# Kernel tuning notes

Measured on AMD Instinct MI355X. Metric: run time of the kernel, lower is better.

## Reference

```python
import jax, jax.numpy as jnp
import numpy as np

VOCAB = 32000
N = 4096        # reservoir_size
D = 32          # avg nonzeros per row -> density D/N
R_OUT = 512
BATCH = 8
T = 256
NNZ = N * D     # W_rec nonzeros = N*N*(D/N)


def setup_inputs() -> dict:
    key = jax.random.key(0)
    ks = jax.random.split(key, 9)
    x = jax.random.randint(ks[0], (BATCH, T), 0, VOCAB)
    # dense input table; sparse.mm(W_in_T, one_hot) == row gather W_in[x_t]
    W_in = jax.random.normal(ks[1], (VOCAB, N), jnp.float32)
    rec_rows = jax.random.randint(ks[2], (NNZ,), 0, N, dtype=jnp.int32)
    rec_cols = jax.random.randint(ks[3], (NNZ,), 0, N, dtype=jnp.int32)
    # small scale stands in for spectral-radius normalization (init-time detail)
    rec_vals = jax.random.normal(ks[4], (NNZ,), jnp.float32) * 0.05
    a = jax.random.uniform(ks[5], (N,), jnp.float32)  # leak rates in [0,1)
    B_w = jax.random.normal(ks[6], (R_OUT, N), jnp.float32) / np.sqrt(N)
    A_w = jax.random.normal(ks[7], (VOCAB, R_OUT), jnp.float32) / np.sqrt(R_OUT)
    A_b = jnp.zeros((VOCAB,), jnp.float32)
    return dict(x=x, W_in=W_in, rec_rows=rec_rows, rec_cols=rec_cols,
                rec_vals=rec_vals, a=a, B_w=B_w, A_w=A_w, A_b=A_b)


def reference(x, W_in, rec_rows, rec_cols, rec_vals, a, B_w, A_w, A_b):
    B = x.shape[0]

    def step(h, x_t):
        # input projection: one-hot @ W_in  ==  row gather
        u = W_in[x_t]                                   # (B, N)
        # sparse COO matvec: rec = W_rec @ h^T, batched over B
        contrib = rec_vals[None, :] * h[:, rec_cols]    # (B, nnz)
        rec = jnp.zeros_like(h).at[:, rec_rows].add(contrib)
        pre = jnp.clip(u + rec, -10.0, 10.0)
        h_new = (1.0 - a) * h + a * jnp.tanh(pre)
        out = (h_new @ B_w.T) @ A_w.T + A_b             # (B, vocab)
        return h_new, out

    h0 = jnp.zeros((B, W_in.shape[1]), W_in.dtype)
    _, outs = jax.lax.scan(step, h0, x.T)               # (T, B, V)
    return jnp.transpose(outs, (1, 0, 2))               # (B, T, V)
```

## Files before the change

kernel.cpp:

```cpp
#include <hip/hip_runtime.h>
#include <hip/hip_bf16.h>
#include <stdint.h>

#define N_RES 4096
#define BATCH 8
#define T_STEPS 256
#define VOCAB 32000
#define R_OUT 512
#define NNZ 131072
#define NNZ_CAP 163840
#define TEAMS 8
#define SLICES 16
#define ROWS_PS 256
#define NWG (TEAMS*SLICES)
#define CSR_CAP 10240

typedef _Float16 v8h __attribute__((ext_vector_type(8)));
typedef float v4f __attribute__((ext_vector_type(4)));

static __device__ __forceinline__ unsigned short f2h(float f) {
    _Float16 h = (_Float16)f;
    unsigned short u;
    __builtin_memcpy(&u, &h, 2);
    return u;
}
static __device__ __forceinline__ float h2f(unsigned short u) {
    _Float16 h;
    __builtin_memcpy(&h, &u, 2);
    return (float)h;
}


#define FLAG_WORDS (TEAMS * SLICES * 32)
#define INIT_WORDS (NNZ_CAP + 4096 + FLAG_WORDS)

__global__ __launch_bounds__(256) void k_init(unsigned* __restrict__ csr,
                                              int* __restrict__ cnt,
                                              unsigned* __restrict__ flags) {
    int i = blockIdx.x * 256 + threadIdx.x;
    if (i < NNZ_CAP) csr[i] = 0u;
    else if (i < NNZ_CAP + 4096) cnt[i - NNZ_CAP] = 0;
    else if (i < INIT_WORDS) flags[i - NNZ_CAP - 4096] = 0u;
}


__global__ __launch_bounds__(256) void k_hist(const int* __restrict__ rows,
                                              int* __restrict__ cnt) {
    int i = blockIdx.x * 256 + threadIdx.x;
    if (i < NNZ) atomicAdd(&cnt[rows[i]], 1);
}

__global__ __launch_bounds__(1024) void k_scan(const int* __restrict__ cnt,
                                               int* __restrict__ row_ptr,
                                               int* __restrict__ cursor) {
    __shared__ int sm[1024];
    int t = threadIdx.x;
    int base = t * 4;
    int c0 = (cnt[base] + 7) & ~7;
    int c1 = (cnt[base + 1] + 7) & ~7;
    int c2 = (cnt[base + 2] + 7) & ~7;
    int c3 = (cnt[base + 3] + 7) & ~7;
    int s = c0 + c1 + c2 + c3;
    sm[t] = s;
    __syncthreads();
    for (int off = 1; off < 1024; off <<= 1) {
        int v = (t >= off) ? sm[t - off] : 0;
        __syncthreads();
        sm[t] += v;
        __syncthreads();
    }
    int run = sm[t] - s;
    row_ptr[base] = run;     cursor[base] = run;     run += c0;
    row_ptr[base + 1] = run; cursor[base + 1] = run; run += c1;
    row_ptr[base + 2] = run; cursor[base + 2] = run; run += c2;
    row_ptr[base + 3] = run; cursor[base + 3] = run; run += c3;
    if (t == 1023) row_ptr[4096] = run;
}

__global__ __launch_bounds__(256) void k_fill(const int* __restrict__ rows,
                                              const int* __restrict__ cols,
                                              const float* __restrict__ vals,
                                              int* __restrict__ cursor,
                                              unsigned* __restrict__ csr) {
    int i = blockIdx.x * 256 + threadIdx.x;
    if (i < NNZ) {
        int r = rows[i];
        int c = cols[i];
        int p = atomicAdd(&cursor[r], 1);
        unsigned off = ((unsigned)(c & 15) << 10) | ((unsigned)(c >> 4) << 2);
        csr[p] = (off << 16) | (unsigned)f2h(vals[i]);
    }
}


#define NB8 (R_OUT * N_RES / 8)
#define NA8 (VOCAB * R_OUT / 8)

__global__ __launch_bounds__(256) void k_cvt2(const float* __restrict__ Bw,
                                              unsigned short* __restrict__ Bwh,
                                              const float* __restrict__ Aw,
                                              unsigned short* __restrict__ Awh) {
    int i = blockIdx.x * 256 + threadIdx.x;
    const float* src;
    unsigned short* dst;
    int j;
    if (i < NB8) { src = Bw; dst = Bwh; j = i * 8; }
    else if (i < NB8 + NA8) { src = Aw; dst = Awh; j = (i - NB8) * 8; }
    else return;
    float4 a0 = *reinterpret_cast<const float4*>(src + j);
    float4 a1 = *reinterpret_cast<const float4*>(src + j + 4);
    unsigned short o[8] = { f2h(a0.x), f2h(a0.y), f2h(a0.z), f2h(a0.w),
                            f2h(a1.x), f2h(a1.y), f2h(a1.z), f2h(a1.w) };
    *reinterpret_cast<uint4*>(dst + j) = *reinterpret_cast<const uint4*>(o);
}


__global__ __launch_bounds__(256) void k_steps(const int* __restrict__ rowptr,
                                               const unsigned* __restrict__ csr,
                                               const float* __restrict__ W_in,
                                               const int* __restrict__ x,
                                               const float* __restrict__ a,
                                               unsigned short* __restrict__ Hb,
                                               unsigned long long* __restrict__ hx,
                                               unsigned* __restrict__ flags) {
    __shared__ float plane[4096];
    __shared__ __align__(16) unsigned lcsr[CSR_CAP];
    __shared__ unsigned long long stage64[64];
    __shared__ int ltok[T_STEPS];

    int wg = blockIdx.x;
    int tid = threadIdx.x;
    int team = wg & 7;
    int slice = wg >> 3;
    int r_own = slice * ROWS_PS + tid;

    ltok[tid] = x[team * T_STEPS + tid];

    int j0 = rowptr[slice * ROWS_PS];
    int j1 = rowptr[slice * ROWS_PS + ROWS_PS];
    int cntE = j1 - j0;
    if (cntE > CSR_CAP) cntE = CSR_CAP;
    {
        const uint4* src = reinterpret_cast<const uint4*>(csr + j0);
        int n4 = cntE >> 2;
        for (int k = tid; k < n4; k += 256)
            reinterpret_cast<uint4*>(lcsr)[k] = src[k];
    }
    for (int k = tid; k < 4096; k += 256) plane[k] = 0.f;

    int js = rowptr[r_own] - j0;
    int je = rowptr[r_own + 1] - j0;
    if (js > CSR_CAP) js = CSR_CAP;
    if (je > CSR_CAP) je = CSR_CAP;
    float av = a[r_own];
    float oma = 1.f - av;
    int pown = ((r_own & 15) << 8) | (r_own >> 4);
    __syncthreads();

    float u_cur = W_in[(size_t)ltok[0] * N_RES + r_own];

    for (int t = 0; t < T_STEPS; ++t) {
        float u_nxt = 0.f;
        if (t + 1 < T_STEPS)
            u_nxt = W_in[(size_t)ltok[t + 1] * N_RES + r_own];

        float acc = 0.f;
        for (int j = js; j < je; j += 8) {
            uint4 e0 = *reinterpret_cast<const uint4*>(lcsr + j);
            uint4 e1 = *reinterpret_cast<const uint4*>(lcsr + j + 4);
            unsigned ee[8] = { e0.x, e0.y, e0.z, e0.w, e1.x, e1.y, e1.z, e1.w };
#pragma unroll
            for (int q = 0; q < 8; ++q) {
                float g = *reinterpret_cast<const float*>(
                    reinterpret_cast<const char*>(plane) + (ee[q] >> 16));
                acc += h2f((unsigned short)(ee[q] & 0xffffu)) * g;
            }
        }
        float hold = plane[pown];
        float pre = u_cur + acc;
        pre = fminf(fmaxf(pre, -10.f), 10.f);
        float ex = __expf(2.f * pre);
        float th = 1.f - 2.f / (ex + 1.f);
        float hv = oma * hold + av * th;
        unsigned short hv16 = f2h(hv);
        Hb[((size_t)(team * T_STEPS + t) << 12) + r_own] = hv16;
        u_cur = u_nxt;

        if (t == T_STEPS - 1) break;

        reinterpret_cast<unsigned short*>(stage64)[tid] = hv16;
        __syncthreads();
        int par = t & 1;
        unsigned long long* base = hx + ((size_t)(par * TEAMS + team)) * 1024;
        if (tid < 64) {
            unsigned long long d = stage64[tid];
            __hip_atomic_store(base + slice * 64 + tid, d,
                               __ATOMIC_RELAXED, __HIP_MEMORY_SCOPE_AGENT);
        }
        asm volatile("s_waitcnt vmcnt(0)" ::: "memory");
        __syncthreads();
        if (tid == 0)
            __hip_atomic_store(flags + (team * SLICES + slice) * 32, (unsigned)(t + 1),
                               __ATOMIC_RELAXED, __HIP_MEMORY_SCOPE_AGENT);
        if (tid < SLICES) {
            const unsigned* fp = flags + (team * SLICES + tid) * 32;
            while (__hip_atomic_load(fp, __ATOMIC_RELAXED,
                                     __HIP_MEMORY_SCOPE_AGENT) < (unsigned)(t + 1)) {}
        }
        __syncthreads();
        const unsigned long long* src = base + tid * 4;
#pragma unroll
        for (int k = 0; k < 4; ++k) {
            unsigned long long d = __hip_atomic_load(src + k, __ATOMIC_RELAXED,
                                                     __HIP_MEMORY_SCOPE_AGENT);
            int jb = k * 4;
            plane[((jb + 0) << 8) | tid] = h2f((unsigned short)(d & 0xffffu));
            plane[((jb + 1) << 8) | tid] = h2f((unsigned short)((d >> 16) & 0xffffu));
            plane[((jb + 2) << 8) | tid] = h2f((unsigned short)((d >> 32) & 0xffffu));
            plane[((jb + 3) << 8) | tid] = h2f((unsigned short)((d >> 48) & 0xffffu));
        }
        __syncthreads();
    }
}


static __device__ __forceinline__ void stage128x32(const _Float16* __restrict__ g,
                                                   int ld, int row0, int k0,
                                                   _Float16* lds, int wave, int lane) {
#pragma unroll
    for (int q = 0; q < 2; ++q) {
        int i = wave * 128 + q * 64 + lane;
        const _Float16* src = g + (size_t)(row0 + (i >> 2)) * ld + k0 + (i & 3) * 8;
        int loff = __builtin_amdgcn_readfirstlane((wave * 128 + q * 64) * 16);
        __builtin_amdgcn_global_load_lds(
            (const __attribute__((address_space(1))) void*)src,
            (__attribute__((address_space(3))) void*)((char*)lds + loff),
            16, 0, 0);
    }
}


__global__ __launch_bounds__(256) void k_gemm1(const _Float16* __restrict__ Hb,
                                               const _Float16* __restrict__ Bwh,
                                               unsigned short* __restrict__ Rbh) {
    __shared__ _Float16 As[2][128 * 32];
    __shared__ _Float16 Bs[2][128 * 32];
    int tid = threadIdx.x, lane = tid & 63, wave = tid >> 6;
    int wm = wave >> 1, wn = wave & 1;
    int col0 = blockIdx.x * 128;
    int row0 = blockIdx.y * 128;
    int rA = lane & 15, kA = (lane >> 4) * 8;
    v4f acc[4][4];
#pragma unroll
    for (int s = 0; s < 4; ++s)
#pragma unroll
        for (int f = 0; f < 4; ++f) acc[s][f] = (v4f){0.f, 0.f, 0.f, 0.f};

    stage128x32(Hb,  N_RES, row0, 0, As[0], wave, lane);
    stage128x32(Bwh, N_RES, col0, 0, Bs[0], wave, lane);
    const int NIT = N_RES / 32;
    for (int it = 0; it < NIT; ++it) {
        int cur = it & 1;
        __syncthreads();
        asm volatile("s_waitcnt vmcnt(0)" ::: "memory");
        __syncthreads();
        if (it + 1 < NIT) {
            stage128x32(Hb,  N_RES, row0, (it + 1) * 32, As[cur ^ 1], wave, lane);
            stage128x32(Bwh, N_RES, col0, (it + 1) * 32, Bs[cur ^ 1], wave, lane);
        }
        v8h af[4], bf[4];
#pragma unroll
        for (int s = 0; s < 4; ++s)
            af[s] = *reinterpret_cast<const v8h*>(&As[cur][(wm * 64 + s * 16 + rA) * 32 + kA]);
#pragma unroll
        for (int f = 0; f < 4; ++f)
            bf[f] = *reinterpret_cast<const v8h*>(&Bs[cur][(wn * 64 + f * 16 + rA) * 32 + kA]);
#pragma unroll
        for (int s = 0; s < 4; ++s)
#pragma unroll
            for (int f = 0; f < 4; ++f)
                acc[s][f] = __builtin_amdgcn_mfma_f32_16x16x32_f16(af[s], bf[f], acc[s][f], 0, 0, 0);
    }
#pragma unroll
    for (int f = 0; f < 4; ++f) {
        int col = col0 + wn * 64 + f * 16 + (lane & 15);
#pragma unroll
        for (int s = 0; s < 4; ++s)
#pragma unroll
            for (int r = 0; r < 4; ++r) {
                int row = row0 + wm * 64 + s * 16 + (lane >> 4) * 4 + r;
                Rbh[(size_t)row * R_OUT + col] = f2h(acc[s][f][r]);
            }
    }
}


__global__ __launch_bounds__(256) void k_gemm2(const _Float16* __restrict__ Rbh,
                                               const _Float16* __restrict__ Awh,
                                               const float* __restrict__ Ab,
                                               float* __restrict__ out) {
    __shared__ _Float16 As[2][128 * 32];
    __shared__ _Float16 Bs[2][128 * 32];
    int tid = threadIdx.x, lane = tid & 63, wave = tid >> 6;
    int wm = wave >> 1, wn = wave & 1;
    int col0 = blockIdx.x * 128;
    int row0 = blockIdx.y * 128;
    int rA = lane & 15, kA = (lane >> 4) * 8;
    v4f acc[4][4];
#pragma unroll
    for (int s = 0; s < 4; ++s)
#pragma unroll
        for (int f = 0; f < 4; ++f) acc[s][f] = (v4f){0.f, 0.f, 0.f, 0.f};

    stage128x32(Rbh, R_OUT, row0, 0, As[0], wave, lane);
    stage128x32(Awh, R_OUT, col0, 0, Bs[0], wave, lane);
    const int NIT = R_OUT / 32;
    for (int it = 0; it < NIT; ++it) {
        int cur = it & 1;
        __syncthreads();
        asm volatile("s_waitcnt vmcnt(0)" ::: "memory");
        __syncthreads();
        if (it + 1 < NIT) {
            stage128x32(Rbh, R_OUT, row0, (it + 1) * 32, As[cur ^ 1], wave, lane);
            stage128x32(Awh, R_OUT, col0, (it + 1) * 32, Bs[cur ^ 1], wave, lane);
        }
        v8h af[4], bf[4];
#pragma unroll
        for (int s = 0; s < 4; ++s)
            af[s] = *reinterpret_cast<const v8h*>(&As[cur][(wm * 64 + s * 16 + rA) * 32 + kA]);
#pragma unroll
        for (int f = 0; f < 4; ++f)
            bf[f] = *reinterpret_cast<const v8h*>(&Bs[cur][(wn * 64 + f * 16 + rA) * 32 + kA]);
#pragma unroll
        for (int s = 0; s < 4; ++s)
#pragma unroll
            for (int f = 0; f < 4; ++f)
                acc[s][f] = __builtin_amdgcn_mfma_f32_16x16x32_f16(af[s], bf[f], acc[s][f], 0, 0, 0);
    }
#pragma unroll
    for (int f = 0; f < 4; ++f) {
        float bias = Ab[col0 + wn * 64 + f * 16 + (lane & 15)];
#pragma unroll
        for (int s = 0; s < 4; ++s)
#pragma unroll
            for (int r = 0; r < 4; ++r) acc[s][f][r] += bias;
    }
    float* Ct = (float*)As;
#pragma unroll
    for (int s = 0; s < 4; ++s) {
        __syncthreads();
#pragma unroll
        for (int f = 0; f < 4; ++f) {
            int lc = wn * 64 + f * 16 + (lane & 15);
            int lr = wm * 16 + (lane >> 4) * 4;
#pragma unroll
            for (int r = 0; r < 4; ++r)
                Ct[(lr + r) * 128 + lc] = acc[s][f][r];
        }
        __syncthreads();
        int lr2 = tid >> 3;
        int lc2 = (tid & 7) * 16;
        int grow = row0 + (lr2 & 15) + (lr2 >> 4) * 64 + s * 16;
        float* dst = out + (size_t)grow * VOCAB + col0 + lc2;
        const float* srcl = &Ct[lr2 * 128 + lc2];
#pragma unroll
        for (int v = 0; v < 4; ++v)
            *reinterpret_cast<float4*>(dst + v * 4) =
                *reinterpret_cast<const float4*>(srcl + v * 4);
    }
}


extern "C" void kernel_launch(void* const* d_in, const int* in_sizes, int n_in,
                              void* d_out, int out_size, void* d_ws, size_t ws_size,
                              hipStream_t stream) {
    const int*   x        = (const int*)d_in[0];
    const float* W_in     = (const float*)d_in[1];
    const int*   rec_rows = (const int*)d_in[2];
    const int*   rec_cols = (const int*)d_in[3];
    const float* rec_vals = (const float*)d_in[4];
    const float* a        = (const float*)d_in[5];
    const float* B_w      = (const float*)d_in[6];
    const float* A_w      = (const float*)d_in[7];
    const float* A_b      = (const float*)d_in[8];
    float* out = (float*)d_out;

    char* w = (char*)d_ws;
    size_t off = 0;
    auto alloc = [&](size_t bytes) { void* p = w + off; off = (off + bytes + 255) & ~(size_t)255; return p; };

    unsigned short* Hb     = (unsigned short*)alloc((size_t)2048 * N_RES * 2);
    unsigned short* Rbh    = (unsigned short*)alloc((size_t)2048 * R_OUT * 2);
    unsigned short* Bwh    = (unsigned short*)alloc((size_t)R_OUT * N_RES * 2);
    unsigned short* Awh    = (unsigned short*)alloc((size_t)VOCAB * R_OUT * 2);
    unsigned*       csr    = (unsigned*)alloc((size_t)NNZ_CAP * 4);
    int*            rowptr = (int*)alloc(4097 * 4);
    int*            cnt    = (int*)alloc(4096 * 4);
    int*            cursor = (int*)alloc(4096 * 4);
    unsigned long long* hx = (unsigned long long*)alloc(2 * TEAMS * 1024 * 8);
    unsigned*       flags  = (unsigned*)alloc(FLAG_WORDS * 4);

    k_init<<<(INIT_WORDS + 255) / 256, 256, 0, stream>>>(csr, cnt, flags);

    k_hist<<<(NNZ + 255) / 256, 256, 0, stream>>>(rec_rows, cnt);
    k_scan<<<1, 1024, 0, stream>>>(cnt, rowptr, cursor);
    k_fill<<<(NNZ + 255) / 256, 256, 0, stream>>>(rec_rows, rec_cols, rec_vals, cursor, csr);

    k_cvt2<<<(NB8 + NA8 + 255) / 256, 256, 0, stream>>>(B_w, Bwh, A_w, Awh);

    k_steps<<<NWG, 256, 0, stream>>>(rowptr, csr, W_in, x, a, Hb, hx, flags);

    k_gemm1<<<dim3(R_OUT / 128, 2048 / 128), 256, 0, stream>>>(
        (const _Float16*)Hb, (const _Float16*)Bwh, Rbh);
    k_gemm2<<<dim3(VOCAB / 128, 2048 / 128), 256, 0, stream>>>(
        (const _Float16*)Rbh, (const _Float16*)Awh, A_b, out);
}
```

Baseline: 1.342 ms.

## Replace flag barrier with epoch-tagged per-element exchange and XCD-local team mapping

Removes the per-step flag store/spin barrier and staging through LDS. Each thread instead publishes its h value tagged with the step epoch into two buffers: one written at workgroup scope and polled with sc0 loads, and one written at agent scope that serves as a fallback after repeated polling failures. Workgroups are remapped so a team's slices are contiguous block IDs, presumably to place them on the same XCD and share its L2, and the plane layout becomes linear. The fast path depends on hardware scheduling placing a team's blocks on one XCD, so correctness of the workgroup-scope path leans on that placement and on the fallback.

```diff
diff --git a/kernel.cpp b/kernel.cpp
--- a/kernel.cpp
+++ b/kernel.cpp
@@ -31,16 +31,18 @@
 }
 
 
-#define FLAG_WORDS (TEAMS * SLICES * 32)
-#define INIT_WORDS (NNZ_CAP + 4096 + FLAG_WORDS)
+#define HX_WORDS (2 * TEAMS * 4096)
+#define INIT_WORDS (NNZ_CAP + 4096 + 2 * HX_WORDS)
 
 __global__ __launch_bounds__(256) void k_init(unsigned* __restrict__ csr,
                                               int* __restrict__ cnt,
-                                              unsigned* __restrict__ flags) {
+                                              unsigned* __restrict__ hxL,
+                                              unsigned* __restrict__ hxG) {
     int i = blockIdx.x * 256 + threadIdx.x;
     if (i < NNZ_CAP) csr[i] = 0u;
     else if (i < NNZ_CAP + 4096) cnt[i - NNZ_CAP] = 0;
-    else if (i < INIT_WORDS) flags[i - NNZ_CAP - 4096] = 0u;
+    else if (i < NNZ_CAP + 4096 + HX_WORDS) hxL[i - NNZ_CAP - 4096] = 0u;
+    else if (i < INIT_WORDS) hxG[i - NNZ_CAP - 4096 - HX_WORDS] = 0u;
 }
 
 
@@ -85,9 +87,8 @@
     int i = blockIdx.x * 256 + threadIdx.x;
     if (i < NNZ) {
         int r = rows[i];
-        int c = cols[i];
+        unsigned off = (unsigned)(cols[i] << 2);
         int p = atomicAdd(&cursor[r], 1);
-        unsigned off = ((unsigned)(c & 15) << 10) | ((unsigned)(c >> 4) << 2);
         csr[p] = (off << 16) | (unsigned)f2h(vals[i]);
     }
 }
@@ -121,19 +122,20 @@
                                                const int* __restrict__ x,
                                                const float* __restrict__ a,
                                                unsigned short* __restrict__ Hb,
-                                               unsigned long long* __restrict__ hx,
-                                               unsigned* __restrict__ flags) {
+                                               unsigned* __restrict__ hxL,
+                                               unsigned* __restrict__ hxG) {
     __shared__ float plane[4096];
     __shared__ __align__(16) unsigned lcsr[CSR_CAP];
-    __shared__ unsigned long long stage64[64];
     __shared__ int ltok[T_STEPS];
+    __shared__ int s_fb;
 
     int wg = blockIdx.x;
     int tid = threadIdx.x;
-    int team = wg & 7;
-    int slice = wg >> 3;
+    int team = wg >> 4;
+    int slice = wg & 15;
     int r_own = slice * ROWS_PS + tid;
 
+    if (tid == 0) s_fb = 0;
     ltok[tid] = x[team * T_STEPS + tid];
 
     int j0 = rowptr[slice * ROWS_PS];
@@ -154,7 +156,6 @@
     if (je > CSR_CAP) je = CSR_CAP;
     float av = a[r_own];
     float oma = 1.f - av;
-    int pown = ((r_own & 15) << 8) | (r_own >> 4);
     __syncthreads();
 
     float u_cur = W_in[(size_t)ltok[0] * N_RES + r_own];
@@ -176,7 +177,7 @@
                 acc += h2f((unsigned short)(ee[q] & 0xffffu)) * g;
             }
         }
-        float hold = plane[pown];
+        float hold = plane[r_own];
         float pre = u_cur + acc;
         pre = fminf(fmaxf(pre, -10.f), 10.f);
         float ex = __expf(2.f * pre);
@@ -188,36 +189,76 @@
 
         if (t == T_STEPS - 1) break;
 
-        reinterpret_cast<unsigned short*>(stage64)[tid] = hv16;
-        __syncthreads();
-        int par = t & 1;
-        unsigned long long* base = hx + ((size_t)(par * TEAMS + team)) * 1024;
-        if (tid < 64) {
-            unsigned long long d = stage64[tid];
-            __hip_atomic_store(base + slice * 64 + tid, d,
-                               __ATOMIC_RELAXED, __HIP_MEMORY_SCOPE_AGENT);
-        }
-        asm volatile("s_waitcnt vmcnt(0)" ::: "memory");
-        __syncthreads();
-        if (tid == 0)
-            __hip_atomic_store(flags + (team * SLICES + slice) * 32, (unsigned)(t + 1),
-                               __ATOMIC_RELAXED, __HIP_MEMORY_SCOPE_AGENT);
-        if (tid < SLICES) {
-            const unsigned* fp = flags + (team * SLICES + tid) * 32;
-            while (__hip_atomic_load(fp, __ATOMIC_RELAXED,
-                                     __HIP_MEMORY_SCOPE_AGENT) < (unsigned)(t + 1)) {}
-        }
-        __syncthreads();
-        const unsigned long long* src = base + tid * 4;
-#pragma unroll
-        for (int k = 0; k < 4; ++k) {
-            unsigned long long d = __hip_atomic_load(src + k, __ATOMIC_RELAXED,
-                                                     __HIP_MEMORY_SCOPE_AGENT);
-            int jb = k * 4;
-            plane[((jb + 0) << 8) | tid] = h2f((unsigned short)(d & 0xffffu));
-            plane[((jb + 1) << 8) | tid] = h2f((unsigned short)((d >> 16) & 0xffffu));
-            plane[((jb + 2) << 8) | tid] = h2f((unsigned short)((d >> 32) & 0xffffu));
-            plane[((jb + 3) << 8) | tid] = h2f((unsigned short)((d >> 48) & 0xffffu));
+        unsigned e = (unsigned)(t + 1);
+        size_t pofs = (((size_t)(e & 1u) * TEAMS + team) << 12);
+        unsigned tagged = (e << 16) | (unsigned)hv16;
+
+        __hip_atomic_store(hxL + pofs + r_own, tagged,
+                           __ATOMIC_RELAXED, __HIP_MEMORY_SCOPE_WORKGROUP);
+        __hip_atomic_store(hxG + pofs + r_own, tagged,
+                           __ATOMIC_RELAXED, __HIP_MEMORY_SCOPE_AGENT);
+
+        unsigned long long g[8];
+        bool fb = (s_fb != 0);
+#define TAGOK64(v) ((((unsigned)((v) >> 16) & 0xffffu) == e) && ((unsigned)((v) >> 48) == e))
+        if (!fb) {
+            uint4 q0, q1, q2, q3;
+            const char* pL = reinterpret_cast<const char*>(hxL + pofs) + (size_t)tid * 64;
+            int tries = 0;
+            for (;;) {
+                asm volatile("global_load_dwordx4 %0, %1, off sc0"
+                             : "=v"(q0) : "v"(pL) : "memory");
+                asm volatile("global_load_dwordx4 %0, %1, off offset:16 sc0"
+                             : "=v"(q1) : "v"(pL) : "memory");
+                asm volatile("global_load_dwordx4 %0, %1, off offset:32 sc0"
+                             : "=v"(q2) : "v"(pL) : "memory");
+                asm volatile("global_load_dwordx4 %0, %1, off offset:48 sc0"
+                             : "=v"(q3) : "v"(pL) : "memory");
+                asm volatile("s_waitcnt vmcnt(0)" ::: "memory");
+                g[0] = (unsigned long long)q0.x | ((unsigned long long)q0.y << 32);
+                g[1] = (unsigned long long)q0.z | ((unsigned long long)q0.w << 32);
+                g[2] = (unsigned long long)q1.x | ((unsigned long long)q1.y << 32);
+                g[3] = (unsigned long long)q1.z | ((unsigned long long)q1.w << 32);
+                g[4] = (unsigned long long)q2.x | ((unsigned long long)q2.y << 32);
+                g[5] = (unsigned long long)q2.z | ((unsigned long long)q2.w << 32);
+                g[6] = (unsigned long long)q3.x | ((unsigned long long)q3.y << 32);
+                g[7] = (unsigned long long)q3.z | ((unsigned long long)q3.w << 32);
+                bool ok = true;
+#pragma unroll
+                for (int k = 0; k < 8; ++k) ok = ok && TAGOK64(g[k]);
+                if (ok) break;
+                if (++tries > 256) { fb = true; s_fb = 1; break; }
+            }
+        }
+        if (fb) {
+            const unsigned long long* xG64 =
+                reinterpret_cast<const unsigned long long*>(hxG + pofs) + (size_t)tid * 8;
+#pragma unroll
+            for (int k = 0; k < 8; ++k)
+                g[k] = __hip_atomic_load(xG64 + k, __ATOMIC_RELAXED,
+                                         __HIP_MEMORY_SCOPE_AGENT);
+            for (;;) {
+                unsigned m = 0;
+#pragma unroll
+                for (int k = 0; k < 8; ++k)
+                    m |= TAGOK64(g[k]) ? 0u : (1u << k);
+                if (!m) break;
+#pragma unroll
+                for (int k = 0; k < 8; ++k)
+                    if (m & (1u << k))
+                        g[k] = __hip_atomic_load(xG64 + k, __ATOMIC_RELAXED,
+                                                 __HIP_MEMORY_SCOPE_AGENT);
+            }
+        }
+#undef TAGOK64
+
+        __syncthreads();
+#pragma unroll
+        for (int k = 0; k < 8; ++k) {
+            float2 v;
+            v.x = h2f((unsigned short)(g[k] & 0xffffu));
+            v.y = h2f((unsigned short)((g[k] >> 32) & 0xffffu));
+            *reinterpret_cast<float2*>(&plane[16 * tid + 2 * k]) = v;
         }
         __syncthreads();
     }
@@ -397,10 +438,10 @@
     int*            rowptr = (int*)alloc(4097 * 4);
     int*            cnt    = (int*)alloc(4096 * 4);
     int*            cursor = (int*)alloc(4096 * 4);
-    unsigned long long* hx = (unsigned long long*)alloc(2 * TEAMS * 1024 * 8);
-    unsigned*       flags  = (unsigned*)alloc(FLAG_WORDS * 4);
-
-    k_init<<<(INIT_WORDS + 255) / 256, 256, 0, stream>>>(csr, cnt, flags);
+    unsigned*       hxL    = (unsigned*)alloc((size_t)HX_WORDS * 4);
+    unsigned*       hxG    = (unsigned*)alloc((size_t)HX_WORDS * 4);
+
+    k_init<<<(INIT_WORDS + 255) / 256, 256, 0, stream>>>(csr, cnt, hxL, hxG);
 
     k_hist<<<(NNZ + 255) / 256, 256, 0, stream>>>(rec_rows, cnt);
     k_scan<<<1, 1024, 0, stream>>>(cnt, rowptr, cursor);
@@ -408,7 +449,7 @@
 
     k_cvt2<<<(NB8 + NA8 + 255) / 256, 256, 0, stream>>>(B_w, Bwh, A_w, Awh);
 
-    k_steps<<<NWG, 256, 0, stream>>>(rowptr, csr, W_in, x, a, Hb, hx, flags);
+    k_steps<<<NWG, 256, 0, stream>>>(rowptr, csr, W_in, x, a, Hb, hxL, hxG);
 
     k_gemm1<<<dim3(R_OUT / 128, 2048 / 128), 256, 0, stream>>>(
         (const _Float16*)Hb, (const _Float16*)Bwh, Rbh);
```

Result: slower. 1.787 ms (+33.2%).

## Tag exchanged hidden state with epoch and shrink gemm1 tiles

Applied to the files above, without the earlier changes.

The recurrent step exchange now writes each element as a 32-bit word that packs an epoch tag with the fp16 value, straight from every thread. This drops the LDS staging, the vmcnt drain and one barrier before the flag store. Readers use sc0 sc1 dwordx4 loads and retry until every tag matches the current epoch, with an atomic fallback after a bounded number of retries. The exchange buffer doubles in size and the plane layout is remapped to match. Separately, gemm1 tiles shrink from 128x128 to 64x64, giving 256 workgroups instead of 64 so more CUs are busy, at the cost of less data reuse per tile.

```diff
diff --git a/kernel.cpp b/kernel.cpp
--- a/kernel.cpp
+++ b/kernel.cpp
@@ -121,11 +121,10 @@
                                                const int* __restrict__ x,
                                                const float* __restrict__ a,
                                                unsigned short* __restrict__ Hb,
-                                               unsigned long long* __restrict__ hx,
+                                               unsigned* __restrict__ hx,
                                                unsigned* __restrict__ flags) {
     __shared__ float plane[4096];
     __shared__ __align__(16) unsigned lcsr[CSR_CAP];
-    __shared__ unsigned long long stage64[64];
     __shared__ int ltok[T_STEPS];
 
     int wg = blockIdx.x;
@@ -183,42 +182,84 @@
         float th = 1.f - 2.f / (ex + 1.f);
         float hv = oma * hold + av * th;
         unsigned short hv16 = f2h(hv);
+
+        if (t == T_STEPS - 1) {
+            Hb[((size_t)(team * T_STEPS + t) << 12) + r_own] = hv16;
+            break;
+        }
+
+        unsigned e = (unsigned)(t + 1);
+        unsigned* xb = hx + (((size_t)(e & 1u) * TEAMS + team) << 12);
+
+        __hip_atomic_store(xb + r_own, (e << 16) | (unsigned)hv16,
+                           __ATOMIC_RELAXED, __HIP_MEMORY_SCOPE_AGENT);
+        __syncthreads();
+        if (tid == 0)
+            __hip_atomic_store(flags + (team * SLICES + slice) * 32, e,
+                               __ATOMIC_RELAXED, __HIP_MEMORY_SCOPE_AGENT);
+
         Hb[((size_t)(team * T_STEPS + t) << 12) + r_own] = hv16;
-        u_cur = u_nxt;
-
-        if (t == T_STEPS - 1) break;
-
-        reinterpret_cast<unsigned short*>(stage64)[tid] = hv16;
-        __syncthreads();
-        int par = t & 1;
-        unsigned long long* base = hx + ((size_t)(par * TEAMS + team)) * 1024;
-        if (tid < 64) {
-            unsigned long long d = stage64[tid];
-            __hip_atomic_store(base + slice * 64 + tid, d,
-                               __ATOMIC_RELAXED, __HIP_MEMORY_SCOPE_AGENT);
-        }
-        asm volatile("s_waitcnt vmcnt(0)" ::: "memory");
-        __syncthreads();
-        if (tid == 0)
-            __hip_atomic_store(flags + (team * SLICES + slice) * 32, (unsigned)(t + 1),
-                               __ATOMIC_RELAXED, __HIP_MEMORY_SCOPE_AGENT);
+
         if (tid < SLICES) {
             const unsigned* fp = flags + (team * SLICES + tid) * 32;
             while (__hip_atomic_load(fp, __ATOMIC_RELAXED,
-                                     __HIP_MEMORY_SCOPE_AGENT) < (unsigned)(t + 1)) {}
-        }
-        __syncthreads();
-        const unsigned long long* src = base + tid * 4;
-#pragma unroll
-        for (int k = 0; k < 4; ++k) {
-            unsigned long long d = __hip_atomic_load(src + k, __ATOMIC_RELAXED,
-                                                     __HIP_MEMORY_SCOPE_AGENT);
-            int jb = k * 4;
-            plane[((jb + 0) << 8) | tid] = h2f((unsigned short)(d & 0xffffu));
-            plane[((jb + 1) << 8) | tid] = h2f((unsigned short)((d >> 16) & 0xffffu));
-            plane[((jb + 2) << 8) | tid] = h2f((unsigned short)((d >> 32) & 0xffffu));
-            plane[((jb + 3) << 8) | tid] = h2f((unsigned short)((d >> 48) & 0xffffu));
-        }
+                                     __HIP_MEMORY_SCOPE_AGENT) < e) {}
+        }
+        __syncthreads();
+
+        uint4 v0, v1, v2, v3;
+        const char* p0 = reinterpret_cast<const char*>(xb) + (size_t)tid * 16;
+        const char* p1 = p0 + 4096;
+        const char* p2 = p0 + 8192;
+        const char* p3 = p0 + 12288;
+        asm volatile(
+            "global_load_dwordx4 %0, %4, off sc0 sc1\n\t"
+            "global_load_dwordx4 %1, %5, off sc0 sc1\n\t"
+            "global_load_dwordx4 %2, %6, off sc0 sc1\n\t"
+            "global_load_dwordx4 %3, %7, off sc0 sc1\n\t"
+            "s_waitcnt vmcnt(0)"
+            : "=&v"(v0), "=&v"(v1), "=&v"(v2), "=&v"(v3)
+            : "v"(p0), "v"(p1), "v"(p2), "v"(p3)
+            : "memory");
+#define QOK(v) (((v.x >> 16) == e) && ((v.y >> 16) == e) && \
+                ((v.z >> 16) == e) && ((v.w >> 16) == e))
+        int tries = 0;
+        while (!(QOK(v0) && QOK(v1) && QOK(v2) && QOK(v3)) && tries <= 64) {
+            ++tries;
+            if (!QOK(v0)) asm volatile("global_load_dwordx4 %0, %1, off sc0 sc1\n\ts_waitcnt vmcnt(0)" : "=&v"(v0) : "v"(p0) : "memory");
+            if (!QOK(v1)) asm volatile("global_load_dwordx4 %0, %1, off sc0 sc1\n\ts_waitcnt vmcnt(0)" : "=&v"(v1) : "v"(p1) : "memory");
+            if (!QOK(v2)) asm volatile("global_load_dwordx4 %0, %1, off sc0 sc1\n\ts_waitcnt vmcnt(0)" : "=&v"(v2) : "v"(p2) : "memory");
+            if (!QOK(v3)) asm volatile("global_load_dwordx4 %0, %1, off sc0 sc1\n\ts_waitcnt vmcnt(0)" : "=&v"(v3) : "v"(p3) : "memory");
+        }
+        if (tries > 64) {
+            unsigned w[16];
+#pragma unroll
+            for (int k = 0; k < 16; ++k) {
+                const unsigned* wp = xb + (k >> 2) * 1024 + tid * 4 + (k & 3);
+                unsigned g = __hip_atomic_load(wp, __ATOMIC_RELAXED, __HIP_MEMORY_SCOPE_AGENT);
+                while ((g >> 16) != e)
+                    g = __hip_atomic_load(wp, __ATOMIC_RELAXED, __HIP_MEMORY_SCOPE_AGENT);
+                w[k] = g;
+            }
+            v0 = (uint4){w[0], w[1], w[2], w[3]};
+            v1 = (uint4){w[4], w[5], w[6], w[7]};
+            v2 = (uint4){w[8], w[9], w[10], w[11]};
+            v3 = (uint4){w[12], w[13], w[14], w[15]};
+        }
+#undef QOK
+        {
+            unsigned wv[16] = { v0.x, v0.y, v0.z, v0.w, v1.x, v1.y, v1.z, v1.w,
+                                v2.x, v2.y, v2.z, v2.w, v3.x, v3.y, v3.z, v3.w };
+#pragma unroll
+            for (int q = 0; q < 4; ++q)
+#pragma unroll
+                for (int i = 0; i < 4; ++i) {
+                    int r = (q << 10) + 4 * tid + i;
+                    plane[((r & 15) << 8) | (r >> 4)] =
+                        h2f((unsigned short)(wv[q * 4 + i] & 0xffffu));
+                }
+        }
+        u_cur = u_nxt;
         __syncthreads();
     }
 }
@@ -239,25 +280,37 @@
     }
 }
 
+static __device__ __forceinline__ void stage64x32(const _Float16* __restrict__ g,
+                                                  int ld, int row0, int k0,
+                                                  _Float16* lds, int wave, int lane) {
+    int i = wave * 64 + lane;
+    const _Float16* src = g + (size_t)(row0 + (i >> 2)) * ld + k0 + (i & 3) * 8;
+    int loff = __builtin_amdgcn_readfirstlane(wave * 64 * 16);
+    __builtin_amdgcn_global_load_lds(
+        (const __attribute__((address_space(1))) void*)src,
+        (__attribute__((address_space(3))) void*)((char*)lds + loff),
+        16, 0, 0);
+}
+
 
 __global__ __launch_bounds__(256) void k_gemm1(const _Float16* __restrict__ Hb,
                                                const _Float16* __restrict__ Bwh,
                                                unsigned short* __restrict__ Rbh) {
-    __shared__ _Float16 As[2][128 * 32];
-    __shared__ _Float16 Bs[2][128 * 32];
+    __shared__ _Float16 As[2][64 * 32];
+    __shared__ _Float16 Bs[2][64 * 32];
     int tid = threadIdx.x, lane = tid & 63, wave = tid >> 6;
     int wm = wave >> 1, wn = wave & 1;
-    int col0 = blockIdx.x * 128;
-    int row0 = blockIdx.y * 128;
+    int col0 = blockIdx.x * 64;
+    int row0 = blockIdx.y * 64;
     int rA = lane & 15, kA = (lane >> 4) * 8;
-    v4f acc[4][4];
-#pragma unroll
-    for (int s = 0; s < 4; ++s)
-#pragma unroll
-        for (int f = 0; f < 4; ++f) acc[s][f] = (v4f){0.f, 0.f, 0.f, 0.f};
-
-    stage128x32(Hb,  N_RES, row0, 0, As[0], wave, lane);
-    stage128x32(Bwh, N_RES, col0, 0, Bs[0], wave, lane);
+    v4f acc[2][2];
+#pragma unroll
+    for (int s = 0; s < 2; ++s)
+#pragma unroll
+        for (int f = 0; f < 2; ++f) acc[s][f] = (v4f){0.f, 0.f, 0.f, 0.f};
+
+    stage64x32(Hb,  N_RES, row0, 0, As[0], wave, lane);
+    stage64x32(Bwh, N_RES, col0, 0, Bs[0], wave, lane);
     const int NIT = N_RES / 32;
     for (int it = 0; it < NIT; ++it) {
         int cur = it & 1;
@@ -265,30 +318,30 @@
         asm volatile("s_waitcnt vmcnt(0)" ::: "memory");
         __syncthreads();
         if (it + 1 < NIT) {
-            stage128x32(Hb,  N_RES, row0, (it + 1) * 32, As[cur ^ 1], wave, lane);
-            stage128x32(Bwh, N_RES, col0, (it + 1) * 32, Bs[cur ^ 1], wave, lane);
-        }
-        v8h af[4], bf[4];
-#pragma unroll
-        for (int s = 0; s < 4; ++s)
-            af[s] = *reinterpret_cast<const v8h*>(&As[cur][(wm * 64 + s * 16 + rA) * 32 + kA]);
-#pragma unroll
-        for (int f = 0; f < 4; ++f)
-            bf[f] = *reinterpret_cast<const v8h*>(&Bs[cur][(wn * 64 + f * 16 + rA) * 32 + kA]);
-#pragma unroll
-        for (int s = 0; s < 4; ++s)
-#pragma unroll
-            for (int f = 0; f < 4; ++f)
+            stage64x32(Hb,  N_RES, row0, (it + 1) * 32, As[cur ^ 1], wave, lane);
+            stage64x32(Bwh, N_RES, col0, (it + 1) * 32, Bs[cur ^ 1], wave, lane);
+        }
+        v8h af[2], bf[2];
+#pragma unroll
+        for (int s = 0; s < 2; ++s)
+            af[s] = *reinterpret_cast<const v8h*>(&As[cur][(wm * 32 + s * 16 + rA) * 32 + kA]);
+#pragma unroll
+        for (int f = 0; f < 2; ++f)
+            bf[f] = *reinterpret_cast<const v8h*>(&Bs[cur][(wn * 32 + f * 16 + rA) * 32 + kA]);
+#pragma unroll
+        for (int s = 0; s < 2; ++s)
+#pragma unroll
+            for (int f = 0; f < 2; ++f)
                 acc[s][f] = __builtin_amdgcn_mfma_f32_16x16x32_f16(af[s], bf[f], acc[s][f], 0, 0, 0);
     }
 #pragma unroll
-    for (int f = 0; f < 4; ++f) {
-        int col = col0 + wn * 64 + f * 16 + (lane & 15);
-#pragma unroll
-        for (int s = 0; s < 4; ++s)
-#pragma unroll
-            for (int r = 0; r < 4; ++r) {
-                int row = row0 + wm * 64 + s * 16 + (lane >> 4) * 4 + r;
+    for (int f = 0; f < 2; ++f) {
+        int col = col0 + wn * 32 + f * 16 + (lane & 15);
+#pragma unroll
+        for (int s = 0; s < 2; ++s)
+#pragma unroll
+            for (int r = 0; r < 2 * 2; ++r) {
+                int row = row0 + wm * 32 + s * 16 + (lane >> 4) * 4 + r;
                 Rbh[(size_t)row * R_OUT + col] = f2h(acc[s][f][r]);
             }
     }
@@ -397,7 +450,7 @@
     int*            rowptr = (int*)alloc(4097 * 4);
     int*            cnt    = (int*)alloc(4096 * 4);
     int*            cursor = (int*)alloc(4096 * 4);
-    unsigned long long* hx = (unsigned long long*)alloc(2 * TEAMS * 1024 * 8);
+    unsigned*       hx     = (unsigned*)alloc((size_t)2 * TEAMS * 4096 * 4);
     unsigned*       flags  = (unsigned*)alloc(FLAG_WORDS * 4);
 
     k_init<<<(INIT_WORDS + 255) / 256, 256, 0, stream>>>(csr, cnt, flags);
@@ -410,7 +463,7 @@
 
     k_steps<<<NWG, 256, 0, stream>>>(rowptr, csr, W_in, x, a, Hb, hx, flags);
 
-    k_gemm1<<<dim3(R_OUT / 128, 2048 / 128), 256, 0, stream>>>(
+    k_gemm1<<<dim3(R_OUT / 64, 2048 / 64), 256, 0, stream>>>(
         (const _Float16*)Hb, (const _Float16*)Bwh, Rbh);
     k_gemm2<<<dim3(VOCAB / 128, 2048 / 128), 256, 0, stream>>>(
         (const _Float16*)Rbh, (const _Float16*)Awh, A_b, out);
```

After: 1.280 ms. 1.05x faster.
